# Kernel tuning notes

Measured on AMD Instinct MI355X. Metric: run time of the kernel, lower is better.

Reference implementation:

```python
import jax, jax.numpy as jnp
import numpy as np

DIM = 1024
H = 16
DH = 64
INNER = H * DH
SCALE = DH ** -0.5


def setup_inputs() -> dict:
    key = jax.random.key(0)
    ks = jax.random.split(key, 6)
    B, L, R = 4, 4096, 512
    x = jax.random.normal(ks[0], (B, L, DIM), dtype=jnp.float32)
    context = jax.random.normal(ks[1], (B, R, DIM), dtype=jnp.float32)
    s = DIM ** -0.5
    Wq = jax.random.normal(ks[2], (DIM, INNER), dtype=jnp.float32) * s
    Wk = jax.random.normal(ks[3], (DIM, INNER), dtype=jnp.float32) * s
    Wv = jax.random.normal(ks[4], (DIM, INNER), dtype=jnp.float32) * s
    Wo = jax.random.normal(ks[5], (INNER, DIM), dtype=jnp.float32) * (INNER ** -0.5)
    return {"x": x, "context": context, "Wq": Wq, "Wk": Wk, "Wv": Wv, "Wo": Wo}


def reference(x, context, Wq, Wk, Wv, Wo):
    B, L, _ = x.shape
    R = context.shape[1]
    # project and split heads: (B, H, L/R, Dh)
    q = (x @ Wq).reshape(B, L, H, DH).transpose(0, 2, 1, 3)
    k = (context @ Wk).reshape(B, R, H, DH).transpose(0, 2, 1, 3)
    v = (context @ Wv).reshape(B, R, H, DH).transpose(0, 2, 1, 3)
    scores = jnp.einsum('bhld,bhrd->bhlr', q, k) * SCALE  # (B,H,L,R)
    attn = jax.nn.softmax(scores, axis=-1)
    out = jnp.einsum('bhlr,bhrd->bhld', attn, v)
    out = out.transpose(0, 2, 1, 3).reshape(B, L, INNER)
    return out @ Wo
```

## Files before the change

kernel.cpp:

```cpp
#include <hip/hip_runtime.h>
#include <hip/hip_bf16.h>

#define DIMC 1024
#define HEADS 16
#define DHEAD 64
#define LQ 4096
#define RK 512
#define BATCH 4

#define QSCALE 0.18033688011112042f

using bf16x8  = __attribute__((ext_vector_type(8))) __bf16;
using short4v = __attribute__((ext_vector_type(4))) short;
using f32x4   = __attribute__((ext_vector_type(4))) float;

__device__ inline ushort f2bf(float f) {
  __hip_bfloat16 h = __float2bfloat16(f);
  return *reinterpret_cast<ushort*>(&h);
}

__device__ inline float exp2_fast(float x) {
  float r; asm("v_exp_f32 %0, %1" : "=v"(r) : "v"(x)); return r;
}

__global__ __launch_bounds__(256) void cvt_in(const float* __restrict__ x,
    const float* __restrict__ ctx, ushort* __restrict__ xb,
    ushort* __restrict__ ctxb) {
  size_t i = ((size_t)blockIdx.x * 256 + threadIdx.x) * 8;
  const float* src; ushort* dst; size_t off;
  if (i < (size_t)16777216) { src = x; dst = xb; off = i; }
  else { src = ctx; dst = ctxb; off = i - 16777216; }
  float4 a = *(const float4*)(src + off);
  float4 b = *(const float4*)(src + off + 4);
  ushort u[8];
  u[0]=f2bf(a.x); u[1]=f2bf(a.y); u[2]=f2bf(a.z); u[3]=f2bf(a.w);
  u[4]=f2bf(b.x); u[5]=f2bf(b.y); u[6]=f2bf(b.z); u[7]=f2bf(b.w);
  *(uint4*)(dst + off) = *(const uint4*)u;
}

__global__ __launch_bounds__(256) void transpose_w(const float* __restrict__ W0,
    const float* __restrict__ W1, const float* __restrict__ W2,
    const float* __restrict__ W3, ushort* __restrict__ D0,
    ushort* __restrict__ D1, ushort* __restrict__ D2, ushort* __restrict__ D3) {
  __shared__ ushort tile[32][33];
  const float* src = (blockIdx.z == 0) ? W0 : (blockIdx.z == 1) ? W1
                   : (blockIdx.z == 2) ? W2 : W3;
  ushort* dst = (blockIdx.z == 0) ? D0 : (blockIdx.z == 1) ? D1
              : (blockIdx.z == 2) ? D2 : D3;
  const int tx = threadIdx.x, ty = threadIdx.y;
  const int x = blockIdx.x * 32 + tx;
  #pragma unroll
  for (int j = 0; j < 32; j += 8)
    tile[ty + j][tx] = f2bf(src[(size_t)(blockIdx.y * 32 + ty + j) * DIMC + x]);
  __syncthreads();
  const int xo = blockIdx.y * 32 + tx;
  #pragma unroll
  for (int j = 0; j < 32; j += 8)
    dst[(size_t)(blockIdx.x * 32 + ty + j) * DIMC + xo] = tile[tx][ty + j];
}

__global__ __launch_bounds__(256) void gemm_bt(const ushort* __restrict__ A,
    const ushort* __restrict__ Bt, void* __restrict__ Cv,
    ushort* __restrict__ CV, int mode) {
  __shared__ ushort As[128 * 32];
  __shared__ ushort Bs[128 * 32];
  const int tid  = threadIdx.x;
  const int wave = tid >> 6, lane = tid & 63;
  const int lr = lane & 15, quad = lane >> 4;
  const int nbx = gridDim.x;
  const int bid = blockIdx.y * nbx + blockIdx.x;
  const int cpx = (nbx * gridDim.y) >> 3;
  const int swz = (bid & 7) * cpx + (bid >> 3);
  const int bx = swz % nbx, by = swz / nbx;
  const size_t m0 = (size_t)by * 128;
  const size_t n0 = (size_t)bx * 128;
  const int wm = (wave >> 1) * 64, wn = (wave & 1) * 64;
  f32x4 acc[4][4] = {};
  for (int k0 = 0; k0 < DIMC; k0 += 32) {
    __syncthreads();
    #pragma unroll
    for (int t = 0; t < 2; ++t) {
      int c = (wave * 2 + t) * 64 + lane;
      int row = c >> 2, cc = c & 3;
      const ushort* ga = A  + (m0 + row) * DIMC + k0 + cc * 8;
      const ushort* gb = Bt + (n0 + row) * DIMC + k0 + cc * 8;
      __builtin_amdgcn_global_load_lds(
          (__attribute__((address_space(1))) void*)ga,
          (__attribute__((address_space(3))) void*)(As + (size_t)(wave * 2 + t) * 512),
          16, 0, 0);
      __builtin_amdgcn_global_load_lds(
          (__attribute__((address_space(1))) void*)gb,
          (__attribute__((address_space(3))) void*)(Bs + (size_t)(wave * 2 + t) * 512),
          16, 0, 0);
    }
    __syncthreads();
    bf16x8 af[4], bfr[4];
    #pragma unroll
    for (int mt = 0; mt < 4; ++mt)
      af[mt] = *(const bf16x8*)(As + (wm + mt * 16 + lr) * 32 + quad * 8);
    #pragma unroll
    for (int nt = 0; nt < 4; ++nt)
      bfr[nt] = *(const bf16x8*)(Bs + (wn + nt * 16 + lr) * 32 + quad * 8);
    #pragma unroll
    for (int mt = 0; mt < 4; ++mt)
      #pragma unroll
      for (int nt = 0; nt < 4; ++nt)
        acc[mt][nt] = __builtin_amdgcn_mfma_f32_16x16x32_bf16(
            af[mt], bfr[nt], acc[mt][nt], 0, 0, 0);
  }
  if (mode == 1) {
    float* C32 = (float*)Cv;
    #pragma unroll
    for (int mt = 0; mt < 4; ++mt)
      #pragma unroll
      for (int nt = 0; nt < 4; ++nt)
        #pragma unroll
        for (int j = 0; j < 4; ++j) {
          size_t m = m0 + wm + mt * 16 + quad * 4 + j;
          size_t n = n0 + wn + nt * 16 + lr;
          C32[m * DIMC + n] = acc[mt][nt][j];
        }
  } else if (mode == 0 || n0 < 1024) {
    const float scl = (mode == 0) ? QSCALE : 1.0f;
    ushort* C16 = (ushort*)Cv;
    #pragma unroll
    for (int mt = 0; mt < 4; ++mt)
      #pragma unroll
      for (int nt = 0; nt < 4; ++nt)
        #pragma unroll
        for (int j = 0; j < 4; ++j) {
          size_t m = m0 + wm + mt * 16 + quad * 4 + j;
          size_t n = n0 + wn + nt * 16 + lr;
          C16[m * DIMC + n] = f2bf(acc[mt][nt][j] * scl);
        }
  } else {
    #pragma unroll
    for (int mt = 0; mt < 4; ++mt)
      #pragma unroll
      for (int nt = 0; nt < 4; ++nt) {
        size_t m = m0 + wm + mt * 16 + quad * 4;
        int hcol = (int)(n0 + wn + nt * 16 + lr) - 1024;
        int h = hcol >> 6, dh = hcol & 63;
        int bb = (int)(m >> 9), r = (int)(m & 511);
        ushort o4[4];
        #pragma unroll
        for (int j = 0; j < 4; ++j) o4[j] = f2bf(acc[mt][nt][j]);
        *(ushort4*)(CV + (((size_t)bb * HEADS + h) * 64 + dh) * RK + r) =
            *(const ushort4*)o4;
      }
  }
}

__global__ __launch_bounds__(256) void attn(ushort* __restrict__ QO,
    const ushort* __restrict__ K, const ushort* __restrict__ Vt) {
  __shared__ __align__(16) ushort Ks[128 * 64];
  __shared__ __align__(16) ushort Vs[64 * 128];
  const int tid  = threadIdx.x;
  const int wave = tid >> 6, lane = tid & 63;
  const int lr = lane & 15, quad = lane >> 4;
  const int b = blockIdx.z, h = blockIdx.y, qb = blockIdx.x;
  const int lsw = (lr & 7) << 3;

  bf16x8 bq[2];
  {
    size_t row = (size_t)b * LQ + qb * 64 + wave * 16 + lr;
    const ushort* qp = QO + row * DIMC + h * DHEAD + quad * 8;
    bq[0] = *(const bf16x8*)(qp);
    bq[1] = *(const bf16x8*)(qp + 32);
  }

  const int krow = tid >> 3, kcol = (tid & 7) * 8;
  const int vrow = tid >> 4, vcol = (tid & 15) * 8;
  const int kwsw = (krow & 7) << 3;
  const int vwsw = (vrow & 7) << 3;
  const ushort* Kbase = K  + ((size_t)b * RK) * DIMC + h * DHEAD;
  const ushort* Vbase = Vt + (((size_t)b * HEADS + h) * 64) * RK;

  uint4 kr0, kr1, kr2, kr3, vr0, vr1, vr2, vr3;
#define LOADK(rc_, i_) \
  (*(const uint4*)(Kbase + (size_t)((rc_) * 128 + (i_) * 32 + krow) * DIMC + kcol))
#define LOADV(rc_, i_) \
  (*(const uint4*)(Vbase + (size_t)((i_) * 16 + vrow) * RK + (rc_) * 128 + vcol))
#define ISSUE(rc_) do {                                      \
    kr0 = LOADK(rc_, 0); kr1 = LOADK(rc_, 1);                \
    kr2 = LOADK(rc_, 2); kr3 = LOADK(rc_, 3);                \
    vr0 = LOADV(rc_, 0); vr1 = LOADV(rc_, 1);                \
    vr2 = LOADV(rc_, 2); vr3 = LOADV(rc_, 3);                \
  } while (0)

  ISSUE(0);

  float mi = -1e30f, li = 0.f;
  f32x4 o[4] = {};

  for (int rc = 0; rc < 4; ++rc) {
    __syncthreads();
    *(uint4*)(Ks + ((((0 * 32 + krow) * 64) + kcol) ^ kwsw)) = kr0;
    *(uint4*)(Ks + ((((1 * 32 + krow) * 64) + kcol) ^ kwsw)) = kr1;
    *(uint4*)(Ks + ((((2 * 32 + krow) * 64) + kcol) ^ kwsw)) = kr2;
    *(uint4*)(Ks + ((((3 * 32 + krow) * 64) + kcol) ^ kwsw)) = kr3;
    *(uint4*)(Vs + ((((0 * 16 + vrow) * 128) + vcol) ^ vwsw)) = vr0;
    *(uint4*)(Vs + ((((1 * 16 + vrow) * 128) + vcol) ^ vwsw)) = vr1;
    *(uint4*)(Vs + ((((2 * 16 + vrow) * 128) + vcol) ^ vwsw)) = vr2;
    *(uint4*)(Vs + ((((3 * 16 + vrow) * 128) + vcol) ^ vwsw)) = vr3;
    __syncthreads();
    if (rc < 3) ISSUE(rc + 1);

    float s[8][4];
    __builtin_amdgcn_s_setprio(1);
    #pragma unroll
    for (int nt = 0; nt < 8; ++nt) {
      f32x4 acc = {};
      acc = __builtin_amdgcn_mfma_f32_16x16x32_bf16(
          *(const bf16x8*)(Ks + ((((nt * 16 + lr) * 64) + quad * 8) ^ lsw)),
          bq[0], acc, 0, 0, 0);
      acc = __builtin_amdgcn_mfma_f32_16x16x32_bf16(
          *(const bf16x8*)(Ks + ((((nt * 16 + lr) * 64) + quad * 8 + 32) ^ lsw)),
          bq[1], acc, 0, 0, 0);
      #pragma unroll
      for (int j = 0; j < 4; ++j) s[nt][j] = acc[j];
    }
    __builtin_amdgcn_s_setprio(0);

    float c0 = s[0][0], c1 = s[0][1], c2 = s[0][2], c3 = s[0][3];
    #pragma unroll
    for (int nt = 1; nt < 8; ++nt) {
      c0 = fmaxf(c0, s[nt][0]); c1 = fmaxf(c1, s[nt][1]);
      c2 = fmaxf(c2, s[nt][2]); c3 = fmaxf(c3, s[nt][3]);
    }
    float cm = fmaxf(fmaxf(c0, c1), fmaxf(c2, c3));
    cm = fmaxf(cm, __shfl_xor(cm, 16));
    cm = fmaxf(cm, __shfl_xor(cm, 32));

    if (!__all(cm - mi <= 8.f)) {
      float mnew = fmaxf(mi, cm);
      float alpha = exp2_fast(mi - mnew);
      mi = mnew;
      li *= alpha;
      float a_bc[4];
      #pragma unroll
      for (int j = 0; j < 4; ++j) a_bc[j] = __shfl(alpha, quad * 4 + j, 16);
      #pragma unroll
      for (int n2 = 0; n2 < 4; ++n2)
        #pragma unroll
        for (int j = 0; j < 4; ++j) o[n2][j] *= a_bc[j];
    }

    short4v pf[8];
    float r0 = 0.f, r1 = 0.f, r2 = 0.f, r3 = 0.f;
    #pragma unroll
    for (int nt = 0; nt < 8; ++nt) {
      float p0 = exp2_fast(s[nt][0] - mi);
      float p1 = exp2_fast(s[nt][1] - mi);
      float p2 = exp2_fast(s[nt][2] - mi);
      float p3 = exp2_fast(s[nt][3] - mi);
      r0 += p0; r1 += p1; r2 += p2; r3 += p3;
      pf[nt][0] = (short)f2bf(p0); pf[nt][1] = (short)f2bf(p1);
      pf[nt][2] = (short)f2bf(p2); pf[nt][3] = (short)f2bf(p3);
    }
    float rs = (r0 + r1) + (r2 + r3);
    rs += __shfl_xor(rs, 16);
    rs += __shfl_xor(rs, 32);
    li += rs;

    __builtin_amdgcn_s_setprio(1);
    #pragma unroll
    for (int kt = 0; kt < 8; ++kt)
      #pragma unroll
      for (int n2 = 0; n2 < 4; ++n2) {
        short4v bv = *(const short4v*)(
            Vs + ((((n2 * 16 + lr) * 128) + kt * 16 + quad * 4) ^ lsw));
        o[n2] = __builtin_amdgcn_mfma_f32_16x16x16bf16_1k(pf[kt], bv, o[n2], 0, 0, 0);
      }
    __builtin_amdgcn_s_setprio(0);
  }
#undef LOADK
#undef LOADV
#undef ISSUE

  float li_bc[4];
  #pragma unroll
  for (int j = 0; j < 4; ++j) li_bc[j] = __shfl(li, quad * 4 + j, 16);
  #pragma unroll
  for (int n2 = 0; n2 < 4; ++n2)
    #pragma unroll
    for (int j = 0; j < 4; ++j) {
      size_t row = (size_t)b * LQ + qb * 64 + wave * 16 + quad * 4 + j;
      QO[row * DIMC + h * DHEAD + n2 * 16 + lr] = f2bf(o[n2][j] / li_bc[j]);
    }
}

extern "C" void kernel_launch(void* const* d_in, const int* in_sizes, int n_in,
                              void* d_out, int out_size, void* d_ws, size_t ws_size,
                              hipStream_t stream) {
  const float* x   = (const float*)d_in[0];
  const float* ctx = (const float*)d_in[1];

  ushort* outs = (ushort*)d_out;
  ushort* xb   = outs;
  ushort* ctxb = outs + (size_t)16777216;
  ushort* WqT  = outs + (size_t)18874368;
  ushort* WkT  = outs + (size_t)19922944;
  ushort* WvT  = outs + (size_t)20971520;
  ushort* Kw   = outs + (size_t)22020096;
  ushort* Vt_g = outs + (size_t)24117248;

  ushort* ws  = (ushort*)d_ws;
  ushort* Qw  = ws;
  ushort* WoT = ws + (size_t)16384 * 1024;

  cvt_in<<<9216, 256, 0, stream>>>(x, ctx, xb, ctxb);
  transpose_w<<<dim3(32, 32, 4), dim3(32, 8), 0, stream>>>(
      (const float*)d_in[2], (const float*)d_in[3], (const float*)d_in[4],
      (const float*)d_in[5], WqT, WkT, WvT, WoT);
  gemm_bt<<<dim3(8, 128), 256, 0, stream>>>(xb,   WqT, Qw, nullptr, 0);
  gemm_bt<<<dim3(16, 16), 256, 0, stream>>>(ctxb, WkT, Kw, Vt_g,    2);
  attn<<<dim3(LQ / 64, HEADS, BATCH), 256, 0, stream>>>(Qw, Kw, Vt_g);
  gemm_bt<<<dim3(8, 128), 256, 0, stream>>>(Qw, WoT, d_out, nullptr, 1);
}
```

Baseline: 345.1 us.

## Merge prep kernels, fuse Q and KV projections, read V directly in attention

Folds the input-conversion and weight-transpose kernels into one launch, and runs the Q and K/V projection GEMMs as a single grid, which cuts launch count and lets the smaller KV GEMM fill gaps. In the attention kernel, V fragments are now read straight from global memory (the pre-transposed layout) instead of being staged through LDS. That frees LDS and removes the V stores to shared memory. The cost is uncoalesced 8-byte global loads inside the PV loop, which rely on cache hits.

```diff
diff --git a/kernel.cpp b/kernel.cpp
--- a/kernel.cpp
+++ b/kernel.cpp
@@ -23,45 +23,144 @@
   float r; asm("v_exp_f32 %0, %1" : "=v"(r) : "v"(x)); return r;
 }
 
-__global__ __launch_bounds__(256) void cvt_in(const float* __restrict__ x,
+__global__ __launch_bounds__(256) void prep(const float* __restrict__ x,
     const float* __restrict__ ctx, ushort* __restrict__ xb,
-    ushort* __restrict__ ctxb) {
-  size_t i = ((size_t)blockIdx.x * 256 + threadIdx.x) * 8;
-  const float* src; ushort* dst; size_t off;
-  if (i < (size_t)16777216) { src = x; dst = xb; off = i; }
-  else { src = ctx; dst = ctxb; off = i - 16777216; }
-  float4 a = *(const float4*)(src + off);
-  float4 b = *(const float4*)(src + off + 4);
-  ushort u[8];
-  u[0]=f2bf(a.x); u[1]=f2bf(a.y); u[2]=f2bf(a.z); u[3]=f2bf(a.w);
-  u[4]=f2bf(b.x); u[5]=f2bf(b.y); u[6]=f2bf(b.z); u[7]=f2bf(b.w);
-  *(uint4*)(dst + off) = *(const uint4*)u;
-}
-
-__global__ __launch_bounds__(256) void transpose_w(const float* __restrict__ W0,
-    const float* __restrict__ W1, const float* __restrict__ W2,
-    const float* __restrict__ W3, ushort* __restrict__ D0,
-    ushort* __restrict__ D1, ushort* __restrict__ D2, ushort* __restrict__ D3) {
+    ushort* __restrict__ ctxb,
+    const float* __restrict__ W0, const float* __restrict__ W1,
+    const float* __restrict__ W2, const float* __restrict__ W3,
+    ushort* __restrict__ D0, ushort* __restrict__ D1,
+    ushort* __restrict__ D2, ushort* __restrict__ D3) {
   __shared__ ushort tile[32][33];
-  const float* src = (blockIdx.z == 0) ? W0 : (blockIdx.z == 1) ? W1
-                   : (blockIdx.z == 2) ? W2 : W3;
-  ushort* dst = (blockIdx.z == 0) ? D0 : (blockIdx.z == 1) ? D1
-              : (blockIdx.z == 2) ? D2 : D3;
-  const int tx = threadIdx.x, ty = threadIdx.y;
-  const int x = blockIdx.x * 32 + tx;
+  const int bid = blockIdx.x;
+  if (bid < 9216) {
+    size_t i = ((size_t)bid * 256 + threadIdx.x) * 8;
+    const float* src; ushort* dst; size_t off;
+    if (i < (size_t)16777216) { src = x; dst = xb; off = i; }
+    else { src = ctx; dst = ctxb; off = i - 16777216; }
+    float4 a = *(const float4*)(src + off);
+    float4 b = *(const float4*)(src + off + 4);
+    ushort u[8];
+    u[0]=f2bf(a.x); u[1]=f2bf(a.y); u[2]=f2bf(a.z); u[3]=f2bf(a.w);
+    u[4]=f2bf(b.x); u[5]=f2bf(b.y); u[6]=f2bf(b.z); u[7]=f2bf(b.w);
+    *(uint4*)(dst + off) = *(const uint4*)u;
+    return;
+  }
+  const int tb = bid - 9216;
+  const int z = tb >> 10, rem = tb & 1023;
+  const int bx = rem & 31, by = rem >> 5;
+  const float* src = (z == 0) ? W0 : (z == 1) ? W1 : (z == 2) ? W2 : W3;
+  ushort* dst = (z == 0) ? D0 : (z == 1) ? D1 : (z == 2) ? D2 : D3;
+  const int tx = threadIdx.x & 31, ty = threadIdx.x >> 5;
+  const int xg = bx * 32 + tx;
   #pragma unroll
   for (int j = 0; j < 32; j += 8)
-    tile[ty + j][tx] = f2bf(src[(size_t)(blockIdx.y * 32 + ty + j) * DIMC + x]);
+    tile[ty + j][tx] = f2bf(src[(size_t)(by * 32 + ty + j) * DIMC + xg]);
   __syncthreads();
-  const int xo = blockIdx.y * 32 + tx;
+  const int xo = by * 32 + tx;
   #pragma unroll
   for (int j = 0; j < 32; j += 8)
-    dst[(size_t)(blockIdx.x * 32 + ty + j) * DIMC + xo] = tile[tx][ty + j];
+    dst[(size_t)(bx * 32 + ty + j) * DIMC + xo] = tile[tx][ty + j];
+}
+
+__global__ __launch_bounds__(256) void gemm_qkv(const ushort* __restrict__ xb,
+    const ushort* __restrict__ ctxb, const ushort* __restrict__ WqT,
+    const ushort* __restrict__ WkvT, ushort* __restrict__ Qw,
+    ushort* __restrict__ Kw, ushort* __restrict__ Vt) {
+  __shared__ ushort As[128 * 32];
+  __shared__ ushort Bs[128 * 32];
+  const int tid  = threadIdx.x;
+  const int wave = tid >> 6, lane = tid & 63;
+  const int lr = lane & 15, quad = lane >> 4;
+  const ushort* A; const ushort* Bt; size_t m0, n0; int seg;
+  if (blockIdx.y < 128) {
+    int bid = blockIdx.y * 8 + blockIdx.x;
+    int swz = (bid & 7) * 128 + (bid >> 3);
+    m0 = (size_t)(swz >> 3) * 128;
+    n0 = (size_t)(swz & 7) * 128;
+    A = xb; Bt = WqT; seg = 0;
+  } else {
+    int bid = (blockIdx.y - 128) * 8 + blockIdx.x;
+    int swz = (bid & 7) * 32 + (bid >> 3);
+    m0 = (size_t)(swz >> 4) * 128;
+    n0 = (size_t)(swz & 15) * 128;
+    A = ctxb; Bt = WkvT; seg = 1;
+  }
+  const int wm = (wave >> 1) * 64, wn = (wave & 1) * 64;
+  f32x4 acc[4][4] = {};
+  for (int k0 = 0; k0 < DIMC; k0 += 32) {
+    __syncthreads();
+    #pragma unroll
+    for (int t = 0; t < 2; ++t) {
+      int c = (wave * 2 + t) * 64 + lane;
+      int row = c >> 2, cc = c & 3;
+      const ushort* ga = A  + (m0 + row) * DIMC + k0 + cc * 8;
+      const ushort* gb = Bt + (n0 + row) * DIMC + k0 + cc * 8;
+      __builtin_amdgcn_global_load_lds(
+          (__attribute__((address_space(1))) void*)ga,
+          (__attribute__((address_space(3))) void*)(As + (size_t)(wave * 2 + t) * 512),
+          16, 0, 0);
+      __builtin_amdgcn_global_load_lds(
+          (__attribute__((address_space(1))) void*)gb,
+          (__attribute__((address_space(3))) void*)(Bs + (size_t)(wave * 2 + t) * 512),
+          16, 0, 0);
+    }
+    __syncthreads();
+    bf16x8 af[4], bfr[4];
+    #pragma unroll
+    for (int mt = 0; mt < 4; ++mt)
+      af[mt] = *(const bf16x8*)(As + (wm + mt * 16 + lr) * 32 + quad * 8);
+    #pragma unroll
+    for (int nt = 0; nt < 4; ++nt)
+      bfr[nt] = *(const bf16x8*)(Bs + (wn + nt * 16 + lr) * 32 + quad * 8);
+    #pragma unroll
+    for (int mt = 0; mt < 4; ++mt)
+      #pragma unroll
+      for (int nt = 0; nt < 4; ++nt)
+        acc[mt][nt] = __builtin_amdgcn_mfma_f32_16x16x32_bf16(
+            af[mt], bfr[nt], acc[mt][nt], 0, 0, 0);
+  }
+  if (seg == 0) {
+    #pragma unroll
+    for (int mt = 0; mt < 4; ++mt)
+      #pragma unroll
+      for (int nt = 0; nt < 4; ++nt)
+        #pragma unroll
+        for (int j = 0; j < 4; ++j) {
+          size_t m = m0 + wm + mt * 16 + quad * 4 + j;
+          size_t n = n0 + wn + nt * 16 + lr;
+          Qw[m * DIMC + n] = f2bf(acc[mt][nt][j] * QSCALE);
+        }
+  } else if (n0 < 1024) {
+    #pragma unroll
+    for (int mt = 0; mt < 4; ++mt)
+      #pragma unroll
+      for (int nt = 0; nt < 4; ++nt)
+        #pragma unroll
+        for (int j = 0; j < 4; ++j) {
+          size_t m = m0 + wm + mt * 16 + quad * 4 + j;
+          size_t n = n0 + wn + nt * 16 + lr;
+          Kw[m * DIMC + n] = f2bf(acc[mt][nt][j]);
+        }
+  } else {
+    #pragma unroll
+    for (int mt = 0; mt < 4; ++mt)
+      #pragma unroll
+      for (int nt = 0; nt < 4; ++nt) {
+        size_t m = m0 + wm + mt * 16 + quad * 4;
+        int hcol = (int)(n0 + wn + nt * 16 + lr) - 1024;
+        int h = hcol >> 6, dh = hcol & 63;
+        int bb = (int)(m >> 9), r = (int)(m & 511);
+        ushort o4[4];
+        #pragma unroll
+        for (int j = 0; j < 4; ++j) o4[j] = f2bf(acc[mt][nt][j]);
+        *(ushort4*)(Vt + (((size_t)bb * HEADS + h) * 64 + dh) * RK + r) =
+            *(const ushort4*)o4;
+      }
+  }
 }
 
 __global__ __launch_bounds__(256) void gemm_bt(const ushort* __restrict__ A,
-    const ushort* __restrict__ Bt, void* __restrict__ Cv,
-    ushort* __restrict__ CV, int mode) {
+    const ushort* __restrict__ Bt, float* __restrict__ C32) {
   __shared__ ushort As[128 * 32];
   __shared__ ushort Bs[128 * 32];
   const int tid  = threadIdx.x;
@@ -108,53 +207,21 @@
         acc[mt][nt] = __builtin_amdgcn_mfma_f32_16x16x32_bf16(
             af[mt], bfr[nt], acc[mt][nt], 0, 0, 0);
   }
-  if (mode == 1) {
-    float* C32 = (float*)Cv;
-    #pragma unroll
-    for (int mt = 0; mt < 4; ++mt)
-      #pragma unroll
-      for (int nt = 0; nt < 4; ++nt)
-        #pragma unroll
-        for (int j = 0; j < 4; ++j) {
-          size_t m = m0 + wm + mt * 16 + quad * 4 + j;
-          size_t n = n0 + wn + nt * 16 + lr;
-          C32[m * DIMC + n] = acc[mt][nt][j];
-        }
-  } else if (mode == 0 || n0 < 1024) {
-    const float scl = (mode == 0) ? QSCALE : 1.0f;
-    ushort* C16 = (ushort*)Cv;
-    #pragma unroll
-    for (int mt = 0; mt < 4; ++mt)
-      #pragma unroll
-      for (int nt = 0; nt < 4; ++nt)
-        #pragma unroll
-        for (int j = 0; j < 4; ++j) {
-          size_t m = m0 + wm + mt * 16 + quad * 4 + j;
-          size_t n = n0 + wn + nt * 16 + lr;
-          C16[m * DIMC + n] = f2bf(acc[mt][nt][j] * scl);
-        }
-  } else {
-    #pragma unroll
-    for (int mt = 0; mt < 4; ++mt)
-      #pragma unroll
-      for (int nt = 0; nt < 4; ++nt) {
-        size_t m = m0 + wm + mt * 16 + quad * 4;
-        int hcol = (int)(n0 + wn + nt * 16 + lr) - 1024;
-        int h = hcol >> 6, dh = hcol & 63;
-        int bb = (int)(m >> 9), r = (int)(m & 511);
-        ushort o4[4];
-        #pragma unroll
-        for (int j = 0; j < 4; ++j) o4[j] = f2bf(acc[mt][nt][j]);
-        *(ushort4*)(CV + (((size_t)bb * HEADS + h) * 64 + dh) * RK + r) =
-            *(const ushort4*)o4;
+  #pragma unroll
+  for (int mt = 0; mt < 4; ++mt)
+    #pragma unroll
+    for (int nt = 0; nt < 4; ++nt)
+      #pragma unroll
+      for (int j = 0; j < 4; ++j) {
+        size_t m = m0 + wm + mt * 16 + quad * 4 + j;
+        size_t n = n0 + wn + nt * 16 + lr;
+        C32[m * DIMC + n] = acc[mt][nt][j];
       }
-  }
 }
 
 __global__ __launch_bounds__(256) void attn(ushort* __restrict__ QO,
     const ushort* __restrict__ K, const ushort* __restrict__ Vt) {
   __shared__ __align__(16) ushort Ks[128 * 64];
-  __shared__ __align__(16) ushort Vs[64 * 128];
   const int tid  = threadIdx.x;
   const int wave = tid >> 6, lane = tid & 63;
   const int lr = lane & 15, quad = lane >> 4;
@@ -170,22 +237,21 @@
   }
 
   const int krow = tid >> 3, kcol = (tid & 7) * 8;
-  const int vrow = tid >> 4, vcol = (tid & 15) * 8;
   const int kwsw = (krow & 7) << 3;
-  const int vwsw = (vrow & 7) << 3;
-  const ushort* Kbase = K  + ((size_t)b * RK) * DIMC + h * DHEAD;
-  const ushort* Vbase = Vt + (((size_t)b * HEADS + h) * 64) * RK;
-
-  uint4 kr0, kr1, kr2, kr3, vr0, vr1, vr2, vr3;
+  const ushort* Kbase = K + ((size_t)b * RK) * DIMC + h * DHEAD;
+
+  const ushort* vbase = Vt + (((size_t)b * HEADS + h) * 64) * RK + quad * 4;
+  const ushort* vb0 = vbase + (size_t)(0 * 16 + lr) * RK;
+  const ushort* vb1 = vbase + (size_t)(1 * 16 + lr) * RK;
+  const ushort* vb2 = vbase + (size_t)(2 * 16 + lr) * RK;
+  const ushort* vb3 = vbase + (size_t)(3 * 16 + lr) * RK;
+
+  uint4 kr0, kr1, kr2, kr3;
 #define LOADK(rc_, i_) \
   (*(const uint4*)(Kbase + (size_t)((rc_) * 128 + (i_) * 32 + krow) * DIMC + kcol))
-#define LOADV(rc_, i_) \
-  (*(const uint4*)(Vbase + (size_t)((i_) * 16 + vrow) * RK + (rc_) * 128 + vcol))
 #define ISSUE(rc_) do {                                      \
     kr0 = LOADK(rc_, 0); kr1 = LOADK(rc_, 1);                \
     kr2 = LOADK(rc_, 2); kr3 = LOADK(rc_, 3);                \
-    vr0 = LOADV(rc_, 0); vr1 = LOADV(rc_, 1);                \
-    vr2 = LOADV(rc_, 2); vr3 = LOADV(rc_, 3);                \
   } while (0)
 
   ISSUE(0);
@@ -199,10 +265,6 @@
     *(uint4*)(Ks + ((((1 * 32 + krow) * 64) + kcol) ^ kwsw)) = kr1;
     *(uint4*)(Ks + ((((2 * 32 + krow) * 64) + kcol) ^ kwsw)) = kr2;
     *(uint4*)(Ks + ((((3 * 32 + krow) * 64) + kcol) ^ kwsw)) = kr3;
-    *(uint4*)(Vs + ((((0 * 16 + vrow) * 128) + vcol) ^ vwsw)) = vr0;
-    *(uint4*)(Vs + ((((1 * 16 + vrow) * 128) + vcol) ^ vwsw)) = vr1;
-    *(uint4*)(Vs + ((((2 * 16 + vrow) * 128) + vcol) ^ vwsw)) = vr2;
-    *(uint4*)(Vs + ((((3 * 16 + vrow) * 128) + vcol) ^ vwsw)) = vr3;
     __syncthreads();
     if (rc < 3) ISSUE(rc + 1);
 
@@ -263,19 +325,22 @@
     rs += __shfl_xor(rs, 32);
     li += rs;
 
+    const int ro = rc * 128;
     __builtin_amdgcn_s_setprio(1);
     #pragma unroll
-    for (int kt = 0; kt < 8; ++kt)
-      #pragma unroll
-      for (int n2 = 0; n2 < 4; ++n2) {
-        short4v bv = *(const short4v*)(
-            Vs + ((((n2 * 16 + lr) * 128) + kt * 16 + quad * 4) ^ lsw));
-        o[n2] = __builtin_amdgcn_mfma_f32_16x16x16bf16_1k(pf[kt], bv, o[n2], 0, 0, 0);
-      }
+    for (int kt = 0; kt < 8; ++kt) {
+      short4v bv0 = *(const short4v*)(vb0 + ro + kt * 16);
+      short4v bv1 = *(const short4v*)(vb1 + ro + kt * 16);
+      short4v bv2 = *(const short4v*)(vb2 + ro + kt * 16);
+      short4v bv3 = *(const short4v*)(vb3 + ro + kt * 16);
+      o[0] = __builtin_amdgcn_mfma_f32_16x16x16bf16_1k(pf[kt], bv0, o[0], 0, 0, 0);
+      o[1] = __builtin_amdgcn_mfma_f32_16x16x16bf16_1k(pf[kt], bv1, o[1], 0, 0, 0);
+      o[2] = __builtin_amdgcn_mfma_f32_16x16x16bf16_1k(pf[kt], bv2, o[2], 0, 0, 0);
+      o[3] = __builtin_amdgcn_mfma_f32_16x16x16bf16_1k(pf[kt], bv3, o[3], 0, 0, 0);
+    }
     __builtin_amdgcn_s_setprio(0);
   }
 #undef LOADK
-#undef LOADV
 #undef ISSUE
 
   float li_bc[4];
@@ -309,12 +374,10 @@
   ushort* Qw  = ws;
   ushort* WoT = ws + (size_t)16384 * 1024;
 
-  cvt_in<<<9216, 256, 0, stream>>>(x, ctx, xb, ctxb);
-  transpose_w<<<dim3(32, 32, 4), dim3(32, 8), 0, stream>>>(
+  prep<<<13312, 256, 0, stream>>>(x, ctx, xb, ctxb,
       (const float*)d_in[2], (const float*)d_in[3], (const float*)d_in[4],
       (const float*)d_in[5], WqT, WkT, WvT, WoT);
-  gemm_bt<<<dim3(8, 128), 256, 0, stream>>>(xb,   WqT, Qw, nullptr, 0);
-  gemm_bt<<<dim3(16, 16), 256, 0, stream>>>(ctxb, WkT, Kw, Vt_g,    2);
+  gemm_qkv<<<dim3(8, 160), 256, 0, stream>>>(xb, ctxb, WqT, WkT, Qw, Kw, Vt_g);
   attn<<<dim3(LQ / 64, HEADS, BATCH), 256, 0, stream>>>(Qw, Kw, Vt_g);
-  gemm_bt<<<dim3(8, 128), 256, 0, stream>>>(Qw, WoT, d_out, nullptr, 1);
-}
+  gemm_bt<<<dim3(8, 128), 256, 0, stream>>>(Qw, WoT, (float*)d_out);
+}
```

After: 497.1 us. 44.1% more time.
